# Performance work log

Measured on AMD Instinct MI355X. Metric: run time of the kernel, lower is better.

The kernel has to match this reference:

```python
import jax, jax.numpy as jnp
import numpy as np

NUM_EMBEDDINGS = 1024
EMBEDDING_DIM = 512
SAMPLE_TOKENS = 4
CODE_DIM = EMBEDDING_DIM // SAMPLE_TOKENS  # 128
COMMITMENT_COST = 0.25


def setup_inputs() -> dict:
    key = jax.random.key(0)
    k1, k2 = jax.random.split(key)
    inputs = jax.random.normal(k1, (16, 1024, EMBEDDING_DIM), dtype=jnp.float32)
    # nn.Embedding weight init: uniform(-1/K, 1/K)
    emb_weight = jax.random.uniform(
        k2, (NUM_EMBEDDINGS, CODE_DIM), dtype=jnp.float32,
        minval=-1.0 / NUM_EMBEDDINGS, maxval=1.0 / NUM_EMBEDDINGS)
    return {"inputs": inputs, "emb_weight": emb_weight}


def reference(inputs, emb_weight):
    input_shape = inputs.shape
    flat = inputs.reshape(-1, CODE_DIM)  # [N, d]
    distances = (jnp.sum(flat * flat, axis=1, keepdims=True)
                 + jnp.sum(emb_weight * emb_weight, axis=1)
                 - 2.0 * jnp.matmul(flat, emb_weight.T))  # [N, K]
    encoding_indices = jnp.argmin(distances, axis=1)  # [N]
    # gather codebook rows instead of one-hot matmul (same math)
    quantized = jnp.take(emb_weight, encoding_indices, axis=0).reshape(input_shape)

    e_latent_loss = jnp.mean((jax.lax.stop_gradient(quantized) - inputs) ** 2)
    q_latent_loss = jnp.mean((quantized - jax.lax.stop_gradient(inputs)) ** 2)
    loss = q_latent_loss + COMMITMENT_COST * e_latent_loss

    # straight-through estimator
    quantized_ste = inputs + jax.lax.stop_gradient(quantized - inputs)

    # avg_probs = mean of one-hot encodings = code-usage histogram / N
    n = flat.shape[0]
    counts = jnp.zeros((NUM_EMBEDDINGS,), dtype=jnp.float32).at[encoding_indices].add(1.0)
    avg_probs = counts / n
    perplexity = jnp.exp(-jnp.sum(avg_probs * jnp.log(avg_probs + 1e-10)))

    return (quantized_ste, loss, perplexity)
```

## Files before the change

### kernel.cpp

```cpp
#include <hip/hip_runtime.h>
#include <cmath>

#define DIM      128
#define NROWS    65536
#define KCODES   1024
#define NELEMS   8388608
#define BAND_INT 12288

typedef __attribute__((ext_vector_type(8))) short  short8;
typedef __attribute__((ext_vector_type(4))) float  f32x4;


__device__ inline unsigned short f2bf(float x) {
    unsigned u = __float_as_uint(x);
    unsigned r = u + 0x7FFFu + ((u >> 16) & 1u);
    return (unsigned short)(r >> 16);
}
__device__ inline float bf2f(unsigned short h) {
    return __uint_as_float(((unsigned)h) << 16);
}

__global__ __launch_bounds__(256) void rowsq_kernel(const float* __restrict__ v,
                                                    float* __restrict__ o, int nrows) {
    const int tid  = threadIdx.x;
    const int sub  = tid >> 5;
    const int lane = tid & 31;
    const int row  = blockIdx.x * 8 + sub;
    if (row >= nrows) return;
    const float4 xv = *(const float4*)(v + (size_t)row * DIM + lane * 4);
    float s = xv.x * xv.x + xv.y * xv.y + xv.z * xv.z + xv.w * xv.w;
    #pragma unroll
    for (int off = 16; off > 0; off >>= 1) s += __shfl_xor(s, off);
    if (lane == 0) o[row] = s;
}

__global__ __launch_bounds__(256) void vq_prep_kernel(
        const float* __restrict__ e, unsigned short* __restrict__ Ews,
        float* __restrict__ Bsq, int* __restrict__ counts, double* __restrict__ sse) {
    const int tid = threadIdx.x;
    {
        const int t  = blockIdx.x * 256 + tid;
        const int c  = t >> 4;
        const int gs = t & 15;
        const int kt = gs >> 2, g = gs & 3;
        const int d0 = gs * 8;
        const float4 v0 = *(const float4*)(e + c * DIM + d0);
        const float4 v1 = *(const float4*)(e + c * DIM + d0 + 4);
        float f[8] = {v0.x, v0.y, v0.z, v0.w, v1.x, v1.y, v1.z, v1.w};
        unsigned short h[8], l[8];
        #pragma unroll
        for (int j = 0; j < 8; ++j) {
            h[j] = f2bf(f[j]);
            l[j] = f2bf(f[j] - bf2f(h[j]));
        }
        const int ct = c >> 4, n = c & 15;
        const int bh = (((ct * 8 + kt) * 16 + n) * 4 + g) * 8;
        const int bl = (((ct * 8 + kt + 4) * 16 + n) * 4 + g) * 8;
        uint4 ph, pl;
        ph.x = h[0] | (h[1] << 16); ph.y = h[2] | (h[3] << 16);
        ph.z = h[4] | (h[5] << 16); ph.w = h[6] | (h[7] << 16);
        pl.x = l[0] | (l[1] << 16); pl.y = l[2] | (l[3] << 16);
        pl.z = l[4] | (l[5] << 16); pl.w = l[6] | (l[7] << 16);
        *(uint4*)&Ews[bh] = ph;
        *(uint4*)&Ews[bl] = pl;
    }
    {
        const int lane = tid & 31;
        #pragma unroll
        for (int r2 = 0; r2 < 2; ++r2) {
            const int row = blockIdx.x * 16 + (tid >> 5) * 2 + r2;
            const float4 xv = *(const float4*)(e + (size_t)row * DIM + lane * 4);
            float s = xv.x * xv.x + xv.y * xv.y + xv.z * xv.z + xv.w * xv.w;
            #pragma unroll
            for (int off = 16; off > 0; off >>= 1) s += __shfl_xor(s, off);
            if (lane == 0) Bsq[row] = s;
        }
    }
    if (blockIdx.x == 0) {
        ((int4*)counts)[tid] = make_int4(0, 0, 0, 0);
        if (tid == 0) *sse = 0.0;
    }
}

template<bool FUSE>
__global__ __launch_bounds__(256) void vq_mfma_kernel(
        const float* __restrict__ x, const float* __restrict__ emb,
        const unsigned short* __restrict__ Ews,
        const float* __restrict__ Asq, const float* __restrict__ Bsq,
        int* __restrict__ idx_out, int* __restrict__ counts,
        double* __restrict__ sse, float* __restrict__ out) {
    __shared__ unsigned short Bs[2][8192];
    __shared__ unsigned short Xs[8192];
    __shared__ float pblk[2];

    const int tid  = threadIdx.x;
    const int wave = tid >> 6;
    const int lane = tid & 63;
    const int n    = lane & 15;
    const int quad = lane >> 4;
    const int row0 = blockIdx.x * 128;

    short8 Af[2][8];
    {
        const int rl    = tid >> 3;
        const int rti   = rl >> 4, m = rl & 15;
        const int dbase = (tid & 7) * 16;
        for (int w = 0; w < 4; ++w) {
            const float* xp = x + (size_t)(row0 + 32 * w + rl) * DIM + dbase;
            #pragma unroll
            for (int q = 0; q < 4; ++q) {
                const float4 v = *(const float4*)(xp + 4 * q);
                const int dd = dbase + 4 * q;
                const int kt = dd >> 5, g = (dd >> 3) & 3, jo = dd & 7;
                unsigned short h0 = f2bf(v.x), h1 = f2bf(v.y), h2 = f2bf(v.z), h3 = f2bf(v.w);
                unsigned short l0 = f2bf(v.x - bf2f(h0)), l1 = f2bf(v.y - bf2f(h1));
                unsigned short l2 = f2bf(v.z - bf2f(h2)), l3 = f2bf(v.w - bf2f(h3));
                uint2 ph, pl;
                ph.x = h0 | (h1 << 16); ph.y = h2 | (h3 << 16);
                pl.x = l0 | (l1 << 16); pl.y = l2 | (l3 << 16);
                const int oh = (((rti * 8 + kt) * 16 + m) * 4 + g) * 8 + jo;
                const int ol = (((rti * 8 + kt + 4) * 16 + m) * 4 + g) * 8 + jo;
                *(uint2*)&Xs[oh] = ph;
                *(uint2*)&Xs[ol] = pl;
            }
            __syncthreads();
            if (wave == w) {
                #pragma unroll
                for (int rt = 0; rt < 2; ++rt)
                    #pragma unroll
                    for (int s8 = 0; s8 < 8; ++s8)
                        Af[rt][s8] = *(const short8*)&Xs[(((rt * 8 + s8) * 16 + n) * 4 + quad) * 8];
            }
            __syncthreads();
        }
    }

    int K1[8], K2[8];
    #pragma unroll
    for (int i = 0; i < 8; ++i) { K1[i] = (int)0x80000000; K2[i] = (int)0x80000000; }

    const uint4* Esrc = (const uint4*)Ews;
    uint4 st[4];
    #pragma unroll
    for (int q = 0; q < 4; ++q) st[q] = Esrc[q * 256 + tid];
    #pragma unroll
    for (int q = 0; q < 4; ++q) *(uint4*)&Bs[0][(q * 256 + tid) * 8] = st[q];
    __syncthreads();

    const f32x4 cinit = {1.0f, 1.0f, 1.0f, 1.0f};
    const f32x4 czero = {0.0f, 0.0f, 0.0f, 0.0f};

    int buf = 0;
    for (int s = 0; s < 32; ++s) {
        if (s < 31) {
            #pragma unroll
            for (int q = 0; q < 4; ++q) st[q] = Esrc[(s + 1) * 1024 + q * 256 + tid];
        }
        #pragma unroll
        for (int cte = 0; cte < 2; ++cte) {
            const int ct = 2 * s + cte;
            const unsigned short* bp = &Bs[buf][cte * 4096];
            short8 Bf[8];
            #pragma unroll
            for (int k8 = 0; k8 < 8; ++k8)
                Bf[k8] = *(const short8*)&bp[((k8 * 16 + n) * 4 + quad) * 8];
            f32x4 a0a = cinit, a0b = czero, a0c = czero;
            f32x4 a1a = cinit, a1b = czero, a1c = czero;
            #pragma unroll
            for (int kt = 0; kt < 4; ++kt) {
                a0a = __builtin_amdgcn_mfma_f32_16x16x32_bf16(Af[0][kt],     Bf[kt],     a0a, 0, 0, 0);
                a1a = __builtin_amdgcn_mfma_f32_16x16x32_bf16(Af[1][kt],     Bf[kt],     a1a, 0, 0, 0);
                a0b = __builtin_amdgcn_mfma_f32_16x16x32_bf16(Af[0][kt + 4], Bf[kt],     a0b, 0, 0, 0);
                a1b = __builtin_amdgcn_mfma_f32_16x16x32_bf16(Af[1][kt + 4], Bf[kt],     a1b, 0, 0, 0);
                a0c = __builtin_amdgcn_mfma_f32_16x16x32_bf16(Af[0][kt],     Bf[kt + 4], a0c, 0, 0, 0);
                a1c = __builtin_amdgcn_mfma_f32_16x16x32_bf16(Af[1][kt],     Bf[kt + 4], a1c, 0, 0, 0);
            }
            #pragma unroll
            for (int r = 0; r < 4; ++r) {
                {
                    const float v = (a0a[r] + a0b[r]) + a0c[r];
                    const int key = (__float_as_int(v) & (int)0xFFFFFFC0) | ct;
                    const int t0 = min(K1[r], key);
                    K1[r] = max(K1[r], key);
                    K2[r] = max(K2[r], t0);
                }
                {
                    const float v = (a1a[r] + a1b[r]) + a1c[r];
                    const int key = (__float_as_int(v) & (int)0xFFFFFFC0) | ct;
                    const int t1 = min(K1[4 + r], key);
                    K1[4 + r] = max(K1[4 + r], key);
                    K2[4 + r] = max(K2[4 + r], t1);
                }
            }
        }
        if (s < 31) {
            #pragma unroll
            for (int q = 0; q < 4; ++q) *(uint4*)&Bs[buf ^ 1][(q * 256 + tid) * 8] = st[q];
        }
        __syncthreads();
        buf ^= 1;
    }

    int* sc   = (int*)&Bs[0][0];
    int* sidx = (int*)&Xs[0];
    #pragma unroll
    for (int r8 = 0; r8 < 8; ++r8) {
        const int lr = 32 * wave + 16 * (r8 >> 2) + quad * 4 + (r8 & 3);
        ((int2*)sc)[lr * 16 + n] = make_int2(K1[r8], K2[r8]);
    }
    __syncthreads();

    if (tid < 128) {
        const int row  = tid;
        const int rowg = row0 + row;
        const int2* ent = (const int2*)sc + row * 16;
        int mx = (int)0x80000000;
        #pragma unroll
        for (int e2 = 0; e2 < 16; ++e2) mx = max(mx, ent[e2].x);
        const int thr = mx - BAND_INT;
        int ck[8];
        int nc = 0;
        #pragma unroll
        for (int e2 = 0; e2 < 16; ++e2) {
            const int2 kk = ent[e2];
            if (kk.x >= thr && nc < 8) ck[nc++] = ((kk.x & 63) << 4) | e2;
            if (kk.y >= thr && nc < 8) ck[nc++] = ((kk.y & 63) << 4) | e2;
        }
        float bd = INFINITY;
        int   bk = 0x7fffffff;
        const float4* xr = (const float4*)(x + (size_t)rowg * DIM);
        const float   aq = Asq[rowg];
        for (int c = 0; c < nc; ++c) {
            const int k = ck[c];
            const float4* er = (const float4*)(emb + (size_t)k * DIM);
            float acc = 0.0f;
            #pragma unroll 4
            for (int dd = 0; dd < 32; ++dd) {
                const float4 xv = xr[dd];
                const float4 ev = er[dd];
                acc += xv.x * ev.x;
                acc += xv.y * ev.y;
                acc += xv.z * ev.z;
                acc += xv.w * ev.w;
            }
            const float t    = aq + Bsq[k];
            const float dist = t - 2.0f * acc;
            if (dist < bd || (dist == bd && k < bk)) { bd = dist; bk = k; }
        }
        if constexpr (!FUSE) idx_out[rowg] = bk;
        sidx[row] = bk;
        atomicAdd(&counts[bk], 1);
        float ss = bd;
        #pragma unroll
        for (int off = 32; off > 0; off >>= 1) ss += __shfl_down(ss, off);
        if (lane == 0) pblk[wave] = ss;
    }
    __syncthreads();
    if (tid == 0) atomicAdd(sse, (double)(pblk[0] + pblk[1]));

    if constexpr (FUSE) {
        #pragma unroll
        for (int i = tid; i < 4096; i += 256) {
            const int row = i >> 5, d4 = i & 31;
            const int k = sidx[row];
            const float4 xv = *((const float4*)(x + (size_t)(row0 + row) * DIM) + d4);
            const float4 qv = *((const float4*)emb + (size_t)k * 32 + d4);
            float4 ov;
            ov.x = xv.x + (qv.x - xv.x);
            ov.y = xv.y + (qv.y - xv.y);
            ov.z = xv.z + (qv.z - xv.z);
            ov.w = xv.w + (qv.w - xv.w);
            *((float4*)out + (size_t)(row0 + row) * 32 + d4) = ov;
        }
    }
}

__global__ __launch_bounds__(256) void vq_epilogue_kernel(
        const float* __restrict__ x, const float* __restrict__ emb,
        const int* __restrict__ idx, float* __restrict__ out) {
    const size_t i4 = (size_t)blockIdx.x * 256 + threadIdx.x;
    const int n  = (int)(i4 >> 5);
    const int d4 = (int)(i4 & 31);
    const int k  = idx[n];
    const float4 xv = ((const float4*)x)[i4];
    const float4 qv = ((const float4*)emb)[(size_t)k * 32 + d4];
    float4 ov;
    ov.x = xv.x + (qv.x - xv.x);
    ov.y = xv.y + (qv.y - xv.y);
    ov.z = xv.z + (qv.z - xv.z);
    ov.w = xv.w + (qv.w - xv.w);
    ((float4*)out)[i4] = ov;
}

__global__ __launch_bounds__(1024) void vq_finalize_kernel(
        const int* __restrict__ counts, const double* __restrict__ sse,
        float* __restrict__ out_tail) {
    __shared__ double red[1024];
    const int t = threadIdx.x;
    const float p = (float)counts[t] * (1.0f / 65536.0f);
    red[t] = (double)p * log((double)p + 1e-10);
    __syncthreads();
    for (int s = 512; s > 0; s >>= 1) {
        if (t < s) red[t] += red[t + s];
        __syncthreads();
    }
    if (t == 0) {
        const float m = (float)(*sse * (1.0 / 8388608.0));
        out_tail[0] = m + 0.25f * m;
        out_tail[1] = (float)exp(-red[0]);
    }
}

extern "C" void kernel_launch(void* const* d_in, const int* in_sizes, int n_in,
                              void* d_out, int out_size, void* d_ws, size_t ws_size,
                              hipStream_t stream) {
    const float* x   = (const float*)d_in[0];
    const float* emb = (const float*)d_in[1];
    float* out = (float*)d_out;

    char*   ws     = (char*)d_ws;
    float*  Bsq    = (float*)(ws + 0);
    int*    counts = (int*)(ws + 4096);
    double* sse    = (double*)(ws + 8192);
    float*  Asq    = (float*)(ws + 16384);

    const bool fuse = (ws_size >= 802816);
    unsigned short* Ews = fuse ? (unsigned short*)(ws + 278528)
                               : (unsigned short*)d_out;
    int* idx = (int*)(ws + 278528);

    vq_prep_kernel<<<64, 256, 0, stream>>>(emb, Ews, Bsq, counts, sse);
    rowsq_kernel<<<8192, 256, 0, stream>>>(x, Asq, NROWS);
    if (fuse) {
        vq_mfma_kernel<true><<<512, 256, 0, stream>>>(x, emb, Ews, Asq, Bsq,
                                                      nullptr, counts, sse, out);
    } else {
        vq_mfma_kernel<false><<<512, 256, 0, stream>>>(x, emb, Ews, Asq, Bsq,
                                                       idx, counts, sse, nullptr);
        vq_epilogue_kernel<<<8192, 256, 0, stream>>>(x, emb, idx, out);
    }
    vq_finalize_kernel<<<1, 1024, 0, stream>>>(counts, sse, out + NELEMS);
}
```

Before: 175.1 us.

## Drop split-bf16 correction terms, stream codebook from global, fuse row norms

The coarse MFMA screening pass now uses only the high bf16 part of inputs and codebook, which cuts the MFMAs per tile from six to two. Codebook fragments are loaded straight from global memory into registers with a two-stage register double buffer, replacing the LDS staging and per-step barriers. Input row norms are computed inside the main kernel during the bf16 conversion, which removes the separate rowsq kernel and the unfused epilogue path. The lower-precision screening may widen the candidate band and send more rows through exact fp32 rechecking, or pick wrong candidates if the band is too narrow.

```diff
diff --git a/kernel.cpp b/kernel.cpp
--- a/kernel.cpp
+++ b/kernel.cpp
@@ -2,8 +2,6 @@
 #include <cmath>
 
 #define DIM      128
-#define NROWS    65536
-#define KCODES   1024
 #define NELEMS   8388608
 #define BAND_INT 12288
 
@@ -16,53 +14,28 @@
     unsigned r = u + 0x7FFFu + ((u >> 16) & 1u);
     return (unsigned short)(r >> 16);
 }
-__device__ inline float bf2f(unsigned short h) {
-    return __uint_as_float(((unsigned)h) << 16);
-}
-
-__global__ __launch_bounds__(256) void rowsq_kernel(const float* __restrict__ v,
-                                                    float* __restrict__ o, int nrows) {
-    const int tid  = threadIdx.x;
-    const int sub  = tid >> 5;
-    const int lane = tid & 31;
-    const int row  = blockIdx.x * 8 + sub;
-    if (row >= nrows) return;
-    const float4 xv = *(const float4*)(v + (size_t)row * DIM + lane * 4);
-    float s = xv.x * xv.x + xv.y * xv.y + xv.z * xv.z + xv.w * xv.w;
-    #pragma unroll
-    for (int off = 16; off > 0; off >>= 1) s += __shfl_xor(s, off);
-    if (lane == 0) o[row] = s;
-}
 
 __global__ __launch_bounds__(256) void vq_prep_kernel(
-        const float* __restrict__ e, unsigned short* __restrict__ Ews,
+        const float* __restrict__ e, unsigned short* __restrict__ Ehi,
         float* __restrict__ Bsq, int* __restrict__ counts, double* __restrict__ sse) {
     const int tid = threadIdx.x;
     {
         const int t  = blockIdx.x * 256 + tid;
         const int c  = t >> 4;
         const int gs = t & 15;
-        const int kt = gs >> 2, g = gs & 3;
+        const int kt = gs >> 2, qd = gs & 3;
         const int d0 = gs * 8;
         const float4 v0 = *(const float4*)(e + c * DIM + d0);
         const float4 v1 = *(const float4*)(e + c * DIM + d0 + 4);
         float f[8] = {v0.x, v0.y, v0.z, v0.w, v1.x, v1.y, v1.z, v1.w};
-        unsigned short h[8], l[8];
-        #pragma unroll
-        for (int j = 0; j < 8; ++j) {
-            h[j] = f2bf(f[j]);
-            l[j] = f2bf(f[j] - bf2f(h[j]));
-        }
+        unsigned short h[8];
+        #pragma unroll
+        for (int j = 0; j < 8; ++j) h[j] = f2bf(f[j]);
         const int ct = c >> 4, n = c & 15;
-        const int bh = (((ct * 8 + kt) * 16 + n) * 4 + g) * 8;
-        const int bl = (((ct * 8 + kt + 4) * 16 + n) * 4 + g) * 8;
-        uint4 ph, pl;
+        uint4 ph;
         ph.x = h[0] | (h[1] << 16); ph.y = h[2] | (h[3] << 16);
         ph.z = h[4] | (h[5] << 16); ph.w = h[6] | (h[7] << 16);
-        pl.x = l[0] | (l[1] << 16); pl.y = l[2] | (l[3] << 16);
-        pl.z = l[4] | (l[5] << 16); pl.w = l[6] | (l[7] << 16);
-        *(uint4*)&Ews[bh] = ph;
-        *(uint4*)&Ews[bl] = pl;
+        *(uint4*)&Ehi[(((ct * 4 + kt) * 64 + qd * 16 + n) * 8)] = ph;
     }
     {
         const int lane = tid & 31;
@@ -82,15 +55,49 @@
     }
 }
 
-template<bool FUSE>
-__global__ __launch_bounds__(256) void vq_mfma_kernel(
+#define LOADPAIR(BUF, P)                                                        \
+    do {                                                                        \
+        const unsigned short* _bp = Ehi + (size_t)(P) * 4096;                   \
+        _Pragma("unroll")                                                       \
+        for (int _c = 0; _c < 2; ++_c)                                          \
+            _Pragma("unroll")                                                   \
+            for (int _kt = 0; _kt < 4; ++_kt)                                   \
+                BUF[_c][_kt] = *(const short8*)&_bp[((_c * 4 + _kt) * 64 + lane) * 8]; \
+    } while (0)
+
+#define COMPUTEPAIR(BUF, P)                                                     \
+    do {                                                                        \
+        _Pragma("unroll")                                                       \
+        for (int _c = 0; _c < 2; ++_c) {                                        \
+            const int _ct = 2 * (P) + _c;                                       \
+            f32x4 _a0 = cinit, _a1 = cinit;                                     \
+            _Pragma("unroll")                                                   \
+            for (int _kt = 0; _kt < 4; ++_kt) {                                 \
+                _a0 = __builtin_amdgcn_mfma_f32_16x16x32_bf16(Af[0][_kt], BUF[_c][_kt], _a0, 0, 0, 0); \
+                _a1 = __builtin_amdgcn_mfma_f32_16x16x32_bf16(Af[1][_kt], BUF[_c][_kt], _a1, 0, 0, 0); \
+            }                                                                   \
+            _Pragma("unroll")                                                   \
+            for (int _r = 0; _r < 4; ++_r) {                                    \
+                const int _k0 = (__float_as_int(_a0[_r]) & (int)0xFFFFFFC0) | _ct; \
+                const int _t0 = min(K1[_r], _k0);                               \
+                K1[_r] = max(K1[_r], _k0);                                      \
+                K2[_r] = max(K2[_r], _t0);                                      \
+                const int _k1 = (__float_as_int(_a1[_r]) & (int)0xFFFFFFC0) | _ct; \
+                const int _t1 = min(K1[4 + _r], _k1);                           \
+                K1[4 + _r] = max(K1[4 + _r], _k1);                              \
+                K2[4 + _r] = max(K2[4 + _r], _t1);                              \
+            }                                                                   \
+        }                                                                       \
+    } while (0)
+
+__global__ __launch_bounds__(256) void vq_main_kernel(
         const float* __restrict__ x, const float* __restrict__ emb,
-        const unsigned short* __restrict__ Ews,
-        const float* __restrict__ Asq, const float* __restrict__ Bsq,
-        int* __restrict__ idx_out, int* __restrict__ counts,
-        double* __restrict__ sse, float* __restrict__ out) {
-    __shared__ unsigned short Bs[2][8192];
-    __shared__ unsigned short Xs[8192];
+        const unsigned short* __restrict__ Ehi, const float* __restrict__ Bsq,
+        int* __restrict__ counts, double* __restrict__ sse,
+        float* __restrict__ out) {
+    __shared__ unsigned short Xs[16384];
+    __shared__ float sAsq[128];
+    __shared__ int   sidx[128];
     __shared__ float pblk[2];
 
     const int tid  = threadIdx.x;
@@ -100,109 +107,63 @@
     const int quad = lane >> 4;
     const int row0 = blockIdx.x * 128;
 
-    short8 Af[2][8];
     {
-        const int rl    = tid >> 3;
-        const int rti   = rl >> 4, m = rl & 15;
-        const int dbase = (tid & 7) * 16;
+        const int rl = tid >> 3, tq = tid & 7;
+        const int dbase = tq * 16;
+        const int rg_lo = rl >> 4, m = rl & 15;
         for (int w = 0; w < 4; ++w) {
-            const float* xp = x + (size_t)(row0 + 32 * w + rl) * DIM + dbase;
+            const int r = 32 * w + rl;
+            const float* xp = x + (size_t)(row0 + r) * DIM + dbase;
+            float p[4];
             #pragma unroll
             for (int q = 0; q < 4; ++q) {
                 const float4 v = *(const float4*)(xp + 4 * q);
+                p[q] = v.x * v.x + v.y * v.y + v.z * v.z + v.w * v.w;
                 const int dd = dbase + 4 * q;
-                const int kt = dd >> 5, g = (dd >> 3) & 3, jo = dd & 7;
+                const int kt = dd >> 5, qd = (dd >> 3) & 3, j = dd & 7;
                 unsigned short h0 = f2bf(v.x), h1 = f2bf(v.y), h2 = f2bf(v.z), h3 = f2bf(v.w);
-                unsigned short l0 = f2bf(v.x - bf2f(h0)), l1 = f2bf(v.y - bf2f(h1));
-                unsigned short l2 = f2bf(v.z - bf2f(h2)), l3 = f2bf(v.w - bf2f(h3));
-                uint2 ph, pl;
+                uint2 ph;
                 ph.x = h0 | (h1 << 16); ph.y = h2 | (h3 << 16);
-                pl.x = l0 | (l1 << 16); pl.y = l2 | (l3 << 16);
-                const int oh = (((rti * 8 + kt) * 16 + m) * 4 + g) * 8 + jo;
-                const int ol = (((rti * 8 + kt + 4) * 16 + m) * 4 + g) * 8 + jo;
-                *(uint2*)&Xs[oh] = ph;
-                *(uint2*)&Xs[ol] = pl;
+                const int rg = w * 2 + rg_lo;
+                *(uint2*)&Xs[(((rg * 4 + kt) * 64 + qd * 16 + m) * 8) + j] = ph;
             }
-            __syncthreads();
-            if (wave == w) {
-                #pragma unroll
-                for (int rt = 0; rt < 2; ++rt)
-                    #pragma unroll
-                    for (int s8 = 0; s8 < 8; ++s8)
-                        Af[rt][s8] = *(const short8*)&Xs[(((rt * 8 + s8) * 16 + n) * 4 + quad) * 8];
-            }
-            __syncthreads();
-        }
-    }
+            #pragma unroll
+            for (int q = 0; q < 4; ++q) p[q] += __shfl_xor(p[q], 4);
+            #pragma unroll
+            for (int q = 0; q < 4; ++q) p[q] += __shfl_xor(p[q], 2);
+            #pragma unroll
+            for (int q = 0; q < 4; ++q) p[q] += __shfl_xor(p[q], 1);
+            const float s = (p[0] + p[2]) + (p[1] + p[3]);
+            if (tq == 0) sAsq[r] = s;
+        }
+    }
+    __syncthreads();
+
+    short8 Af[2][4];
+    #pragma unroll
+    for (int rti = 0; rti < 2; ++rti)
+        #pragma unroll
+        for (int kt = 0; kt < 4; ++kt)
+            Af[rti][kt] = *(const short8*)&Xs[(((wave * 2 + rti) * 4 + kt) * 64 + lane) * 8];
+    __syncthreads();
 
     int K1[8], K2[8];
     #pragma unroll
     for (int i = 0; i < 8; ++i) { K1[i] = (int)0x80000000; K2[i] = (int)0x80000000; }
 
-    const uint4* Esrc = (const uint4*)Ews;
-    uint4 st[4];
-    #pragma unroll
-    for (int q = 0; q < 4; ++q) st[q] = Esrc[q * 256 + tid];
-    #pragma unroll
-    for (int q = 0; q < 4; ++q) *(uint4*)&Bs[0][(q * 256 + tid) * 8] = st[q];
-    __syncthreads();
-
     const f32x4 cinit = {1.0f, 1.0f, 1.0f, 1.0f};
-    const f32x4 czero = {0.0f, 0.0f, 0.0f, 0.0f};
-
-    int buf = 0;
-    for (int s = 0; s < 32; ++s) {
-        if (s < 31) {
-            #pragma unroll
-            for (int q = 0; q < 4; ++q) st[q] = Esrc[(s + 1) * 1024 + q * 256 + tid];
-        }
-        #pragma unroll
-        for (int cte = 0; cte < 2; ++cte) {
-            const int ct = 2 * s + cte;
-            const unsigned short* bp = &Bs[buf][cte * 4096];
-            short8 Bf[8];
-            #pragma unroll
-            for (int k8 = 0; k8 < 8; ++k8)
-                Bf[k8] = *(const short8*)&bp[((k8 * 16 + n) * 4 + quad) * 8];
-            f32x4 a0a = cinit, a0b = czero, a0c = czero;
-            f32x4 a1a = cinit, a1b = czero, a1c = czero;
-            #pragma unroll
-            for (int kt = 0; kt < 4; ++kt) {
-                a0a = __builtin_amdgcn_mfma_f32_16x16x32_bf16(Af[0][kt],     Bf[kt],     a0a, 0, 0, 0);
-                a1a = __builtin_amdgcn_mfma_f32_16x16x32_bf16(Af[1][kt],     Bf[kt],     a1a, 0, 0, 0);
-                a0b = __builtin_amdgcn_mfma_f32_16x16x32_bf16(Af[0][kt + 4], Bf[kt],     a0b, 0, 0, 0);
-                a1b = __builtin_amdgcn_mfma_f32_16x16x32_bf16(Af[1][kt + 4], Bf[kt],     a1b, 0, 0, 0);
-                a0c = __builtin_amdgcn_mfma_f32_16x16x32_bf16(Af[0][kt],     Bf[kt + 4], a0c, 0, 0, 0);
-                a1c = __builtin_amdgcn_mfma_f32_16x16x32_bf16(Af[1][kt],     Bf[kt + 4], a1c, 0, 0, 0);
-            }
-            #pragma unroll
-            for (int r = 0; r < 4; ++r) {
-                {
-                    const float v = (a0a[r] + a0b[r]) + a0c[r];
-                    const int key = (__float_as_int(v) & (int)0xFFFFFFC0) | ct;
-                    const int t0 = min(K1[r], key);
-                    K1[r] = max(K1[r], key);
-                    K2[r] = max(K2[r], t0);
-                }
-                {
-                    const float v = (a1a[r] + a1b[r]) + a1c[r];
-                    const int key = (__float_as_int(v) & (int)0xFFFFFFC0) | ct;
-                    const int t1 = min(K1[4 + r], key);
-                    K1[4 + r] = max(K1[4 + r], key);
-                    K2[4 + r] = max(K2[4 + r], t1);
-                }
-            }
-        }
-        if (s < 31) {
-            #pragma unroll
-            for (int q = 0; q < 4; ++q) *(uint4*)&Bs[buf ^ 1][(q * 256 + tid) * 8] = st[q];
-        }
-        __syncthreads();
-        buf ^= 1;
-    }
-
-    int* sc   = (int*)&Bs[0][0];
-    int* sidx = (int*)&Xs[0];
+
+    short8 BfA[2][4], BfB[2][4];
+    LOADPAIR(BfA, 0);
+    for (int u = 0; u < 16; ++u) {
+        const int pA = 2 * u, pB = 2 * u + 1;
+        LOADPAIR(BfB, pB);
+        COMPUTEPAIR(BfA, pA);
+        if (pA + 2 < 32) LOADPAIR(BfA, pA + 2);
+        COMPUTEPAIR(BfB, pB);
+    }
+
+    int* sc = (int*)&Xs[0];
     #pragma unroll
     for (int r8 = 0; r8 < 8; ++r8) {
         const int lr = 32 * wave + 16 * (r8 >> 2) + quad * 4 + (r8 & 3);
@@ -229,7 +190,7 @@
         float bd = INFINITY;
         int   bk = 0x7fffffff;
         const float4* xr = (const float4*)(x + (size_t)rowg * DIM);
-        const float   aq = Asq[rowg];
+        const float   aq = sAsq[row];
         for (int c = 0; c < nc; ++c) {
             const int k = ck[c];
             const float4* er = (const float4*)(emb + (size_t)k * DIM);
@@ -247,7 +208,6 @@
             const float dist = t - 2.0f * acc;
             if (dist < bd || (dist == bd && k < bk)) { bd = dist; bk = k; }
         }
-        if constexpr (!FUSE) idx_out[rowg] = bk;
         sidx[row] = bk;
         atomicAdd(&counts[bk], 1);
         float ss = bd;
@@ -258,38 +218,19 @@
     __syncthreads();
     if (tid == 0) atomicAdd(sse, (double)(pblk[0] + pblk[1]));
 
-    if constexpr (FUSE) {
-        #pragma unroll
-        for (int i = tid; i < 4096; i += 256) {
-            const int row = i >> 5, d4 = i & 31;
-            const int k = sidx[row];
-            const float4 xv = *((const float4*)(x + (size_t)(row0 + row) * DIM) + d4);
-            const float4 qv = *((const float4*)emb + (size_t)k * 32 + d4);
-            float4 ov;
-            ov.x = xv.x + (qv.x - xv.x);
-            ov.y = xv.y + (qv.y - xv.y);
-            ov.z = xv.z + (qv.z - xv.z);
-            ov.w = xv.w + (qv.w - xv.w);
-            *((float4*)out + (size_t)(row0 + row) * 32 + d4) = ov;
-        }
-    }
-}
-
-__global__ __launch_bounds__(256) void vq_epilogue_kernel(
-        const float* __restrict__ x, const float* __restrict__ emb,
-        const int* __restrict__ idx, float* __restrict__ out) {
-    const size_t i4 = (size_t)blockIdx.x * 256 + threadIdx.x;
-    const int n  = (int)(i4 >> 5);
-    const int d4 = (int)(i4 & 31);
-    const int k  = idx[n];
-    const float4 xv = ((const float4*)x)[i4];
-    const float4 qv = ((const float4*)emb)[(size_t)k * 32 + d4];
-    float4 ov;
-    ov.x = xv.x + (qv.x - xv.x);
-    ov.y = xv.y + (qv.y - xv.y);
-    ov.z = xv.z + (qv.z - xv.z);
-    ov.w = xv.w + (qv.w - xv.w);
-    ((float4*)out)[i4] = ov;
+    #pragma unroll
+    for (int i = tid; i < 4096; i += 256) {
+        const int row = i >> 5, d4 = i & 31;
+        const int k = sidx[row];
+        const float4 xv = *((const float4*)(x + (size_t)(row0 + row) * DIM) + d4);
+        const float4 qv = *((const float4*)emb + (size_t)k * 32 + d4);
+        float4 ov;
+        ov.x = xv.x + (qv.x - xv.x);
+        ov.y = xv.y + (qv.y - xv.y);
+        ov.z = xv.z + (qv.z - xv.z);
+        ov.w = xv.w + (qv.w - xv.w);
+        *((float4*)out + (size_t)(row0 + row) * 32 + d4) = ov;
+    }
 }
 
 __global__ __launch_bounds__(1024) void vq_finalize_kernel(
@@ -318,26 +259,13 @@
     const float* emb = (const float*)d_in[1];
     float* out = (float*)d_out;
 
-    char*   ws     = (char*)d_ws;
-    float*  Bsq    = (float*)(ws + 0);
-    int*    counts = (int*)(ws + 4096);
-    double* sse    = (double*)(ws + 8192);
-    float*  Asq    = (float*)(ws + 16384);
-
-    const bool fuse = (ws_size >= 802816);
-    unsigned short* Ews = fuse ? (unsigned short*)(ws + 278528)
-                               : (unsigned short*)d_out;
-    int* idx = (int*)(ws + 278528);
-
-    vq_prep_kernel<<<64, 256, 0, stream>>>(emb, Ews, Bsq, counts, sse);
-    rowsq_kernel<<<8192, 256, 0, stream>>>(x, Asq, NROWS);
-    if (fuse) {
-        vq_mfma_kernel<true><<<512, 256, 0, stream>>>(x, emb, Ews, Asq, Bsq,
-                                                      nullptr, counts, sse, out);
-    } else {
-        vq_mfma_kernel<false><<<512, 256, 0, stream>>>(x, emb, Ews, Asq, Bsq,
-                                                       idx, counts, sse, nullptr);
-        vq_epilogue_kernel<<<8192, 256, 0, stream>>>(x, emb, idx, out);
-    }
+    char*           ws     = (char*)d_ws;
+    float*          Bsq    = (float*)(ws + 0);
+    int*            counts = (int*)(ws + 4096);
+    double*         sse    = (double*)(ws + 8192);
+    unsigned short* Ehi    = (unsigned short*)(ws + 16384);
+
+    vq_prep_kernel<<<64, 256, 0, stream>>>(emb, Ehi, Bsq, counts, sse);
+    vq_main_kernel<<<512, 256, 0, stream>>>(x, emb, Ehi, Bsq, counts, sse, out);
     vq_finalize_kernel<<<1, 1024, 0, stream>>>(counts, sse, out + NELEMS);
 }
```

Result: faster. 144.8 us (-17.3%).
